# Performance work log

Measured on AMD Instinct MI355X. Metric: run time of the kernel, lower is better.

## Reference

```python
import jax, jax.numpy as jnp
import numpy as np

H, W, C, R, N = 200, 200, 256, 1024, 300


def _mlp(f, W1, b1, W2, b2):
    # Linear -> ReLU -> Linear, applied per pixel
    return jax.nn.relu(f @ W1 + b1) @ W2 + b2


def setup_inputs() -> dict:
    key = jax.random.key(0)
    ks = jax.random.split(key, 16)
    s = 0.02
    inp = {
        'x': jax.random.normal(ks[0], (C, H, W), jnp.float32),
        'masks': jax.random.uniform(ks[1], (H, W, N)) < 0.5,
        'labels': jax.random.randint(ks[2], (N,), 0, 3),  # 0=point,1=line,2=circle
    }
    i = 3
    for p in ('p', 'l', 'c'):
        inp[f'W{p}1'] = s * jax.random.normal(ks[i], (C, R), jnp.float32); i += 1
        inp[f'b{p}1'] = jnp.zeros((R,), jnp.float32)
        inp[f'W{p}2'] = s * jax.random.normal(ks[i], (R, R), jnp.float32); i += 1
        inp[f'b{p}2'] = jnp.zeros((R,), jnp.float32)
    return inp


def reference(x, masks, labels, Wp1, bp1, Wp2, bp2, Wl1, bl1, Wl2, bl2, Wc1, bc1, Wc2, bc2):
    feat = jnp.transpose(x, (1, 2, 0))  # [H, W, C]
    # Apply each label-specific MLP densely over the feature map: [3, H, W, R]
    ys = jnp.stack([
        _mlp(feat, Wp1, bp1, Wp2, bp2),
        _mlp(feat, Wl1, bl1, Wl2, bl2),
        _mlp(feat, Wc1, bc1, Wc2, bc2),
    ], axis=0)
    mf = masks.astype(feat.dtype)                       # [H, W, N]
    sums = jnp.einsum('hwn,khwr->nkr', mf, ys)          # masked sums per node per MLP
    counts = jnp.sum(mf, axis=(0, 1))                   # [N] pixels per mask
    means = sums / counts[:, None, None]                # [N, 3, R]
    # pick the MLP branch matching each node's label -> [N, R]
    return means[jnp.arange(means.shape[0]), labels]
```

## Files before the change

### kernel.cpp

```cpp
#include <hip/hip_runtime.h>

typedef unsigned short u16;
typedef unsigned int   u32;

using bf16x8 = __attribute__((ext_vector_type(8))) __bf16;
using f32x4  = __attribute__((ext_vector_type(4))) float;

__device__ __forceinline__ float bf2f(u16 h){ return __uint_as_float(((u32)h) << 16); }
__device__ __forceinline__ u16 f2bf(float f){
    u32 u = __float_as_uint(f);
    u32 r = u + 0x7FFFu + ((u >> 16) & 1u);
    return (u16)(r >> 16);
}

__device__ __forceinline__ void async16(const void* g, void* l){
    __builtin_amdgcn_global_load_lds(
        (const __attribute__((address_space(1))) unsigned int*)g,
        (__attribute__((address_space(3))) unsigned int*)l, 16, 0, 0);
}
__device__ __forceinline__ bf16x8 cvt8(uint4 v){
    union { uint4 u; bf16x8 b; } c; c.u = v; return c.b;
}

__global__ void probe_and_perm(const void* x, const void* masks, int* flags,
                               const int* labels, int* slot_of_node,
                               int* node_of_slot, int* ovf_flag)
{
    if (blockIdx.x == 0){
        int l = threadIdx.x;
        if (l < 64){
            const u16* hx = (const u16*)x;
            int e0 = (hx[l] >> 7) & 0xFF;
            int e1 = (hx[l + 64] >> 7) & 0xFF;
            unsigned long long b0 = __ballot(e0 >= 100 && e0 <= 140);
            unsigned long long b1 = __ballot(e1 >= 100 && e1 <= 140);
            int cnt = __popcll(b0) + __popcll(b1);
            const u32* w  = (const u32*)masks;
            const u16* hm = (const u16*)masks;
            u32 v = w[l];
            unsigned long long i32bad = __ballot(v > 1u);
            unsigned long long f32bad = __ballot(v != 0u && v != 0x3F800000u);
            u16 h0 = hm[l], h1 = hm[l + 64];
            unsigned long long bfbad =
                __ballot((h0 != 0 && h0 != 0x3F80) || (h1 != 0 && h1 != 0x3F80));
            if (l == 0){
                flags[0] = (cnt >= 100) ? 1 : 0;
                int md = 0;
                if (!i32bad) md = 1; else if (!f32bad) md = 3; else if (!bfbad) md = 2;
                flags[1] = md;
            }
        }
        return;
    }
    __shared__ int lab[300];
    __shared__ unsigned char sp[300];
    int t = threadIdx.x;
    for (int idx = t; idx < 512; idx += 320) node_of_slot[idx] = -1;
    if (t < 300) lab[t] = labels[t];
    __syncthreads();
    int r = 0;
    if (t < 300){
        int k = lab[t];
        for (int j = 0; j < t; j++) r += (lab[j] == k);
        sp[t] = (r >= 128) ? 1 : 0;
    }
    __syncthreads();
    if (t < 300){
        int slot;
        if (!sp[t]) slot = lab[t] * 128 + r;
        else {
            int so = 0;
            for (int j = 0; j < t; j++) so += sp[j];
            slot = 384 + so;
        }
        slot_of_node[t] = slot;
        node_of_slot[slot] = t;
    }
    if (t == 0){
        int tot = 0;
        for (int j = 0; j < 300; j++) tot += sp[j];
        *ovf_flag = tot;
    }
}

__global__ void prep_combo(const void* x,
    const void* w10, const void* w11, const void* w12,
    const void* w20, const void* w21, const void* w22,
    const void* bb10, const void* bb11, const void* bb12,
    const void* bb20, const void* bb21, const void* bb22,
    u16* feat, u16* B1T, u16* W2T, float* b1f, float* b2f, const int* flags)
{
    __shared__ float tile[32][33];
    const int id = blockIdx.x;
    const bool isbf = (flags[0] != 0);
    const int tid = threadIdx.x;
    const int tx = tid & 31, ty = tid >> 5;

    const void* src; u16* d; int I, J, ldd, i0, j0;
    if (id < 10016){
        int fx = id % 1252, fy = id / 1252;
        src = x; d = feat; I = 256; J = 40000; ldd = 256;
        j0 = fx * 32; i0 = fy * 32;
    } else if (id < 10016 + 768){
        int idx = id - 10016;
        int z = idx / 256, r2 = idx % 256;
        src = (z == 0) ? w10 : (z == 1) ? w11 : w12;
        d = B1T + (size_t)z * 1024 * 256;
        I = 256; J = 1024; ldd = 256;
        j0 = (r2 % 32) * 32; i0 = (r2 / 32) * 32;
    } else if (id < 10016 + 768 + 3072){
        int idx = id - 10016 - 768;
        int z = idx / 1024, r2 = idx % 1024;
        src = (z == 0) ? w20 : (z == 1) ? w21 : w22;
        d = W2T + (size_t)z * 1024 * 1024;
        I = 1024; J = 1024; ldd = 1024;
        j0 = (r2 % 32) * 32; i0 = (r2 / 32) * 32;
    } else {
        int idx = (id - 10016 - 768 - 3072) * 256 + tid;
        if (idx < 3072){
            int k = idx >> 10, r2 = idx & 1023;
            const void* p1 = (k == 0) ? bb10 : (k == 1) ? bb11 : bb12;
            const void* p2 = (k == 0) ? bb20 : (k == 1) ? bb21 : bb22;
            b1f[idx] = isbf ? bf2f(((const u16*)p1)[r2]) : ((const float*)p1)[r2];
            b2f[idx] = isbf ? bf2f(((const u16*)p2)[r2]) : ((const float*)p2)[r2];
        }
        return;
    }
    #pragma unroll
    for (int s = 0; s < 32; s += 8){
        int i = i0 + ty + s, j = j0 + tx;
        float v = 0.f;
        if (j < J){
            size_t ix = (size_t)i * J + j;
            v = isbf ? bf2f(((const u16*)src)[ix]) : ((const float*)src)[ix];
        }
        tile[ty + s][tx] = v;
    }
    __syncthreads();
    #pragma unroll
    for (int s = 0; s < 32; s += 8){
        int j = j0 + ty + s, i = i0 + tx;
        d[(size_t)j * ldd + i] = f2bf(tile[tx][ty + s]);
    }
}

__global__ void trans_mask_count(const void* src, u16* dst,
                                 const int* slot_of_node, float* counts,
                                 const int* flags)
{
    constexpr int NN_ = 300, P_ = 40000, LDP = 40064;
    __shared__ u16 tile[128][33];
    __shared__ int slt[32];
    const int p0 = blockIdx.x * 128, n0 = blockIdx.y * 32;
    const int tid = threadIdx.x;
    const int md = flags[1];
    if (tid < 32) slt[tid] = (n0 + tid < NN_) ? slot_of_node[n0 + tid] : -1;

    if (md == 0){
        const unsigned char* s8 = (const unsigned char*)src;
        const int tx = tid & 7, ty = tid >> 3;
        #pragma unroll
        for (int rep = 0; rep < 4; rep++){
            const int p = p0 + rep * 32 + ty;
            const int nb = n0 + tx * 4;
            u32 w = 0;
            if (p < P_){
                if (nb + 3 < NN_)
                    w = *(const u32*)(s8 + (size_t)p * NN_ + nb);
                else {
                    for (int b = 0; b < 4; b++)
                        if (nb + b < NN_)
                            w |= (u32)s8[(size_t)p * NN_ + nb + b] << (8 * b);
                }
            }
            #pragma unroll
            for (int b = 0; b < 4; b++)
                tile[rep * 32 + ty][tx * 4 + b] =
                    ((w >> (8 * b)) & 0xFFu) ? (u16)0x3F80 : (u16)0;
        }
    } else {
        #pragma unroll
        for (int it = 0; it < 16; it++){
            const int e = tid + it * 256;
            const int n_in = e & 31, p_in = e >> 5;
            const int p = p0 + p_in, n = n0 + n_in;
            u16 v = 0;
            if (p < P_ && n < NN_){
                size_t idx = (size_t)p * NN_ + n;
                bool on;
                if (md == 1)      on = ((const int*)src)[idx] != 0;
                else if (md == 2) on = ((const u16*)src)[idx] != 0;
                else              on = ((const float*)src)[idx] != 0.f;
                v = on ? (u16)0x3F80 : (u16)0;
            }
            tile[p_in][n_in] = v;
        }
    }
    __syncthreads();

    #pragma unroll
    for (int half = 0; half < 2; half++){
        const int row = tid >> 3;
        const int pos = (tid & 7) + half * 8;
        const int slot = slt[row];
        if (slot >= 0){
            union { u16 h[8]; uint4 v; } tmp;
            #pragma unroll
            for (int j = 0; j < 8; j++) tmp.h[j] = tile[pos * 8 + j][row];
            *reinterpret_cast<uint4*>(&dst[(size_t)slot * LDP + p0 + pos * 8]) = tmp.v;
        }
    }
    if (tid < 32){
        const int slot = slt[tid];
        if (slot >= 0){
            int c = 0;
            for (int p = 0; p < 128; p++) c += (tile[p][tid] != 0);
            if (c > 0) atomicAdd(&counts[slot], (float)c);
        }
    }
}

template<int MAP>
__global__ __launch_bounds__(256, 2)
void fused_l1_mask(const u16* __restrict__ B1T, const u16* __restrict__ feat,
                   const u16* __restrict__ mfT, const float* __restrict__ b1f,
                   float* __restrict__ sums, const int* __restrict__ skipf)
{
    if constexpr (MAP == 1){ if (*skipf == 0) return; }
    constexpr int PPAD = 40064;
    __shared__ __align__(16) u16 As[32768];
    __shared__ __align__(16) u16 Hs[8192];

    int bx, ts, te;
    if constexpr (MAP == 0){
        const int id = blockIdx.x;
        const int r = id & 7, s = (id >> 3) & 7, g = id >> 6;
        const int combo = g * 8 + r;
        if (combo >= 63) return;
        const int branch = combo / 21, y = combo % 21;
        bx = branch * 8 + s;
        ts = y * 15; te = ts + 15; if (te > 313) te = 313;
    } else {
        bx = blockIdx.x;
        ts = blockIdx.y * 40; te = ts + 40; if (te > 313) te = 313;
        if (ts >= te) return;
    }
    const int m0 = bx * 128;
    const int srow = (MAP == 0) ? ((bx >> 3) * 128) : 384;

    const int tid = threadIdx.x;
    const int wave = tid >> 6, lane = tid & 63;
    const int t = lane & 15, q = lane >> 4;

    {
        const int cr = lane >> 2, cp = lane & 3;
        const int ca = wave * 2, cb = wave * 2 + 1;
        const u16* gA0 = B1T + (size_t)(m0 + ca * 16 + cr) * 256 + cp * 8;
        const u16* gA1 = B1T + (size_t)(m0 + cb * 16 + cr) * 256 + cp * 8;
        #pragma unroll
        for (int kt = 0; kt < 8; kt++){
            async16(gA0 + kt * 32, &As[kt * 4096 + ca * 512]);
            async16(gA1 + kt * 32, &As[kt * 4096 + cb * 512]);
        }
    }

    const u16* mrow = mfT + (size_t)(srow + wave * 32 + t) * PPAD + q * 8;
    const u16* gF   = feat + (size_t)(wave * 32 + t) * 256 + q * 8;
    const float4* bsrc = reinterpret_cast<const float4*>(b1f + m0) + q;

    f32x4 acc2[2][8];
    #pragma unroll
    for (int a = 0; a < 2; a++)
        #pragma unroll
        for (int b = 0; b < 8; b++)
            #pragma unroll
            for (int e = 0; e < 4; e++) acc2[a][b][e] = 0.f;

    uint4 bgv[2];
    #pragma unroll
    for (int ni = 0; ni < 2; ni++)
        bgv[ni] = *reinterpret_cast<const uint4*>(
            gF + (size_t)(ts * 128 + ni * 16) * 256);

    __syncthreads();

#define HWRITE(MOFF) do{                                                      \
    _Pragma("unroll")                                                         \
    for (int mi = 0; mi < 4; mi++){                                           \
        _Pragma("unroll")                                                     \
        for (int i = 0; i < 4; i++){                                          \
            const int m_l = mi * 16 + q * 4 + i;                              \
            _Pragma("unroll")                                                 \
            for (int ni = 0; ni < 2; ni++){                                   \
                const int pin = ni * 16 + t;                                  \
                float v = acc1[(MOFF) + mi][ni][i];                           \
                v = (v > 0.f) ? v : 0.f;                                      \
                const int cg = (pin >> 3) ^ q;                                \
                Hs[wave * 2048 + m_l * 32 + cg * 8 + (pin & 7)] = f2bf(v);    \
            }                                                                 \
        }                                                                     \
    }                                                                         \
}while(0)

#define S2HALF(NOFF) do{                                                      \
    _Pragma("unroll")                                                         \
    for (int lc = 0; lc < 4; lc++){                                           \
        const int hq_ = (q ^ ((t >> 2) & 3)) * 8;                             \
        bf16x8 hb0_ = *reinterpret_cast<const bf16x8*>(                       \
            &Hs[lc * 2048 + (0 * 16 + t) * 32 + hq_]);                        \
        bf16x8 hb1_ = *reinterpret_cast<const bf16x8*>(                       \
            &Hs[lc * 2048 + (1 * 16 + t) * 32 + hq_]);                        \
        bf16x8 hb2_ = *reinterpret_cast<const bf16x8*>(                       \
            &Hs[lc * 2048 + (2 * 16 + t) * 32 + hq_]);                        \
        bf16x8 hb3_ = *reinterpret_cast<const bf16x8*>(                       \
            &Hs[lc * 2048 + (3 * 16 + t) * 32 + hq_]);                        \
        __builtin_amdgcn_s_setprio(1);                                        \
        acc2[0][(NOFF)+0] = __builtin_amdgcn_mfma_f32_16x16x32_bf16(          \
            cvt8(mk[lc][0]), hb0_, acc2[0][(NOFF)+0], 0, 0, 0);               \
        acc2[0][(NOFF)+1] = __builtin_amdgcn_mfma_f32_16x16x32_bf16(          \
            cvt8(mk[lc][0]), hb1_, acc2[0][(NOFF)+1], 0, 0, 0);               \
        acc2[0][(NOFF)+2] = __builtin_amdgcn_mfma_f32_16x16x32_bf16(          \
            cvt8(mk[lc][0]), hb2_, acc2[0][(NOFF)+2], 0, 0, 0);               \
        acc2[0][(NOFF)+3] = __builtin_amdgcn_mfma_f32_16x16x32_bf16(          \
            cvt8(mk[lc][0]), hb3_, acc2[0][(NOFF)+3], 0, 0, 0);               \
        acc2[1][(NOFF)+0] = __builtin_amdgcn_mfma_f32_16x16x32_bf16(          \
            cvt8(mk[lc][1]), hb0_, acc2[1][(NOFF)+0], 0, 0, 0);               \
        acc2[1][(NOFF)+1] = __builtin_amdgcn_mfma_f32_16x16x32_bf16(          \
            cvt8(mk[lc][1]), hb1_, acc2[1][(NOFF)+1], 0, 0, 0);               \
        acc2[1][(NOFF)+2] = __builtin_amdgcn_mfma_f32_16x16x32_bf16(          \
            cvt8(mk[lc][1]), hb2_, acc2[1][(NOFF)+2], 0, 0, 0);               \
        acc2[1][(NOFF)+3] = __builtin_amdgcn_mfma_f32_16x16x32_bf16(          \
            cvt8(mk[lc][1]), hb3_, acc2[1][(NOFF)+3], 0, 0, 0);               \
        __builtin_amdgcn_s_setprio(0);                                        \
    }                                                                         \
}while(0)

    for (int pt = ts; pt < te; ++pt){
        const int p0 = pt * 128;

        f32x4 acc1[8][2];
        #pragma unroll
        for (int mi = 0; mi < 8; mi++){
            float4 bb = bsrc[mi * 4];
            #pragma unroll
            for (int ni = 0; ni < 2; ni++){
                acc1[mi][ni][0] = bb.x; acc1[mi][ni][1] = bb.y;
                acc1[mi][ni][2] = bb.z; acc1[mi][ni][3] = bb.w;
            }
        }

        uint4 mk[4][2];

        #pragma unroll
        for (int kt = 0; kt < 8; ++kt){
            bf16x8 af[8];
            #pragma unroll
            for (int mi = 0; mi < 8; mi++)
                af[mi] = *reinterpret_cast<const bf16x8*>(
                    &As[kt * 4096 + (mi * 16 + t) * 32 + q * 8]);
            uint4 nxt[2];
            if (kt < 7){
                #pragma unroll
                for (int ni = 0; ni < 2; ni++)
                    nxt[ni] = *reinterpret_cast<const uint4*>(
                        gF + (size_t)(p0 + ni * 16) * 256 + (kt + 1) * 32);
            }
            if (kt == 6){
                #pragma unroll
                for (int si = 0; si < 2; si++){
                    mk[0][si] = *reinterpret_cast<const uint4*>(
                        mrow + (size_t)(si * 16) * PPAD + p0 + 0 * 32);
                    mk[1][si] = *reinterpret_cast<const uint4*>(
                        mrow + (size_t)(si * 16) * PPAD + p0 + 1 * 32);
                }
            } else if (kt == 7){
                #pragma unroll
                for (int si = 0; si < 2; si++){
                    mk[2][si] = *reinterpret_cast<const uint4*>(
                        mrow + (size_t)(si * 16) * PPAD + p0 + 2 * 32);
                    mk[3][si] = *reinterpret_cast<const uint4*>(
                        mrow + (size_t)(si * 16) * PPAD + p0 + 3 * 32);
                }
            }
            __builtin_amdgcn_s_setprio(1);
            #pragma unroll
            for (int mi = 0; mi < 8; mi++)
                #pragma unroll
                for (int ni = 0; ni < 2; ni++)
                    acc1[mi][ni] = __builtin_amdgcn_mfma_f32_16x16x32_bf16(
                        af[mi], cvt8(bgv[ni]), acc1[mi][ni], 0, 0, 0);
            __builtin_amdgcn_s_setprio(0);
            if (kt < 7){ bgv[0] = nxt[0]; bgv[1] = nxt[1]; }
        }

        HWRITE(0);
        __syncthreads();

        S2HALF(0);
        __syncthreads();

        HWRITE(4);
        if (pt + 1 < te){
            #pragma unroll
            for (int ni = 0; ni < 2; ni++)
                bgv[ni] = *reinterpret_cast<const uint4*>(
                    gF + (size_t)((pt + 1) * 128 + ni * 16) * 256);
        }
        __syncthreads();

        S2HALF(4);
        __syncthreads();
    }
#undef HWRITE
#undef S2HALF

    #pragma unroll
    for (int si = 0; si < 2; si++){
        #pragma unroll
        for (int i = 0; i < 4; i++){
            const int slot_l = wave * 32 + si * 16 + q * 4 + i;
            #pragma unroll
            for (int ni = 0; ni < 8; ni++){
                const int m_l = ni * 16 + t;
                const float v = acc2[si][ni][i];
                if constexpr (MAP == 0)
                    atomicAdd(sums + (size_t)((bx >> 3) * 128 + slot_l) * 1024
                                   + (bx & 7) * 128 + m_l, v);
                else
                    atomicAdd(sums + (size_t)slot_l * 3072 + bx * 128 + m_l, v);
            }
        }
    }
}

__global__ __launch_bounds__(256)
void l2_gemm(const float* __restrict__ sums3, const float* __restrict__ sumsOvf,
             const float* __restrict__ counts, const u16* __restrict__ W2T,
             const float* __restrict__ b2f, const int* __restrict__ node_of_slot,
             const int* __restrict__ labels, const int* __restrict__ ovfflag,
             void* __restrict__ dout, const int* __restrict__ flags)
{
    const int z = blockIdx.z;
    const int k = (z >= 3) ? z - 3 : z;
    if (z >= 3 && *ovfflag == 0) return;
    const int n0 = blockIdx.x * 128;

    const float* Arow; int astride, slotbase;
    if (z < 3){ Arow = sums3 + (size_t)z * 128 * 1024; astride = 1024; slotbase = z * 128; }
    else      { Arow = sumsOvf + (size_t)k * 1024;     astride = 3072; slotbase = 384; }

    __shared__ __align__(16) u16 As[2][4096];
    __shared__ __align__(16) u16 Bs[2][4096];
    __shared__ float invc[128];

    const int tid  = threadIdx.x;
    const int wave = tid >> 6, lane = tid & 63;
    const int wr = wave >> 1, wc = wave & 1;
    const int t = lane & 15, q = lane >> 4;

    if (tid < 128){
        float c = counts[slotbase + tid];
        invc[tid] = (c > 0.f) ? 1.f / c : 0.f;
    }
    __syncthreads();

    const u16* Bsrc = W2T + (size_t)k * 1024 * 1024;
    const int cr = lane >> 2, cp = lane & 3;
    const int ca = wave * 2, cb = wave * 2 + 1;
    const u16* gB0 = Bsrc + (size_t)(n0 + ca * 16 + cr) * 1024 + cp * 8;
    const u16* gB1 = Bsrc + (size_t)(n0 + cb * 16 + cr) * 1024 + cp * 8;

    const int srow0 = tid >> 2, sq0 = tid & 3;
    const int srow1 = srow0 + 64;

    float4 sv[2][2];

#define L2_LOAD(ktv) do{ \
    const float4* _p0 = reinterpret_cast<const float4*>( \
        Arow + (size_t)srow0 * astride + (ktv) * 32 + sq0 * 8); \
    const float4* _p1 = reinterpret_cast<const float4*>( \
        Arow + (size_t)srow1 * astride + (ktv) * 32 + sq0 * 8); \
    sv[0][0] = _p0[0]; sv[0][1] = _p0[1]; \
    sv[1][0] = _p1[0]; sv[1][1] = _p1[1]; }while(0)
// ... 49 lines not shown
            for (int ni = 0; ni < 4; ni++)
                acc[mi][ni] = __builtin_amdgcn_mfma_f32_16x16x32_bf16(
                    af[mi], bg[ni], acc[mi][ni], 0, 0, 0);
        __builtin_amdgcn_s_setprio(0);
        if (kt < 31) L2_WRITE(buf ^ 1);
        __syncthreads();
        buf ^= 1;
    }
#undef L2_LOAD
#undef L2_WRITE

    const bool outbf = (flags[0] != 0);
    #pragma unroll
    for (int mi = 0; mi < 4; mi++){
        #pragma unroll
        for (int i = 0; i < 4; i++){
            int m_l = wr * 64 + mi * 16 + q * 4 + i;
            int node = node_of_slot[slotbase + m_l];
            bool ok = (node >= 0) && (z < 3 || labels[node] == k);
            if (!ok) continue;
            #pragma unroll
            for (int ni = 0; ni < 4; ni++){
                int n = n0 + wc * 64 + ni * 16 + t;
                float v = acc[mi][ni][i] + b2f[k * 1024 + n];
                size_t oi = (size_t)node * 1024 + n;
                if (outbf) ((u16*)dout)[oi] = f2bf(v);
                else       ((float*)dout)[oi] = v;
            }
        }
    }
}

extern "C" void kernel_launch(void* const* d_in, const int* in_sizes, int n_in,
                              void* d_out, int out_size, void* d_ws, size_t ws_size,
                              hipStream_t stream)
{
    constexpr int C = 256, R = 1024;
    constexpr int PPAD = 40064;
    constexpr int M1 = 3 * R;
    constexpr int SLOTS = 512;

    const void* x      = d_in[0];
    const void* masks  = d_in[1];
    const int*  labels = (const int*)d_in[2];
    (void)in_sizes; (void)n_in; (void)out_size; (void)ws_size;

    char* ws = (char*)d_ws;
    size_t off = 0;
    auto alloc = [&](size_t b)->size_t {
        size_t o = off; off += (b + 255) & ~(size_t)255; return o;
    };

    int*   flags   = (int*)  (ws + alloc(256));
    int*   slotmap = (int*)  (ws + alloc(384 * 4));
    int*   nodemap = (int*)  (ws + alloc(512 * 4));
    int*   ovfflag = (int*)  (ws + alloc(256));
    u16*   feat    = (u16*)  (ws + alloc((size_t)PPAD * C * 2));
    u16*   B1T     = (u16*)  (ws + alloc((size_t)M1 * C * 2));
    float* b1f     = (float*)(ws + alloc((size_t)M1 * 4));
    float* b2f     = (float*)(ws + alloc((size_t)M1 * 4));
    u16*   mfT     = (u16*)  (ws + alloc((size_t)SLOTS * PPAD * 2));
    float* sums3   = (float*)(ws + alloc((size_t)384 * 1024 * 4));
    float* sumsOvf = (float*)(ws + alloc((size_t)128 * M1 * 4));
    float* counts  = (float*)(ws + alloc((size_t)SLOTS * 4));
    u16*   W2T     = (u16*)  (ws + alloc((size_t)3 * R * R * 2));

    probe_and_perm<<<2, 320, 0, stream>>>(x, masks, flags, labels,
                                          slotmap, nodemap, ovfflag);
    hipMemsetAsync(sums3, 0,
        (size_t)384 * 1024 * 4 + (size_t)128 * M1 * 4 + (size_t)SLOTS * 4, stream);

    prep_combo<<<10016 + 768 + 3072 + 12, 256, 0, stream>>>(
        x, d_in[3], d_in[7], d_in[11],
        d_in[5], d_in[9], d_in[13],
        d_in[4], d_in[8], d_in[12],
        d_in[6], d_in[10], d_in[14],
        feat, B1T, W2T, b1f, b2f, flags);

    trans_mask_count<<<dim3(PPAD / 128, 384 / 32), 256, 0, stream>>>(
        masks, mfT, slotmap, counts, flags);

    fused_l1_mask<0><<<512, 256, 0, stream>>>(
        B1T, feat, mfT, b1f, sums3, nullptr);
    fused_l1_mask<1><<<dim3(24, 8), 256, 0, stream>>>(
        B1T, feat, mfT, b1f, sumsOvf, ovfflag);

    l2_gemm<<<dim3(8, 1, 6), 256, 0, stream>>>(
        sums3, sumsOvf, counts, W2T, b2f, nodemap, labels, ovfflag,
        d_out, flags);
}
```

Before: 351.3 us.

## Split fused L1-mask kernel across 8 waves and fold memset into probe kernel

The fused layer-1/mask kernel moves from 4 waves to 8 waves per block, and each wave now owns 16 pixels/slots instead of 32. This halves the per-wave accumulator and register footprint and reworks the LDS layout of the hidden tile with a new XOR swizzle, aiming for higher occupancy (launch bounds 512,4). The software prefetch of features and masks one step ahead is dropped in favour of direct loads, which may expose more memory latency. Separately, the hipMemsetAsync that zeroed the sums buffers is replaced by extra blocks in the probe kernel, removing one launch.

```diff
diff --git a/kernel.cpp b/kernel.cpp
--- a/kernel.cpp
+++ b/kernel.cpp
@@ -24,8 +24,17 @@
 
 __global__ void probe_and_perm(const void* x, const void* masks, int* flags,
                                const int* labels, int* slot_of_node,
-                               int* node_of_slot, int* ovf_flag)
+                               int* node_of_slot, int* ovf_flag,
+                               float* zbuf, unsigned int zf4)
 {
+    if (blockIdx.x >= 2){
+        const unsigned int nthr = (gridDim.x - 2) * blockDim.x;
+        unsigned int i = (blockIdx.x - 2) * blockDim.x + threadIdx.x;
+        float4 z = make_float4(0.f, 0.f, 0.f, 0.f);
+        for (; i < zf4; i += nthr)
+            reinterpret_cast<float4*>(zbuf)[i] = z;
+        return;
+    }
     if (blockIdx.x == 0){
         int l = threadIdx.x;
         if (l < 64){
@@ -221,7 +230,7 @@
 }
 
 template<int MAP>
-__global__ __launch_bounds__(256, 2)
+__global__ __launch_bounds__(512, 4)
 void fused_l1_mask(const u16* __restrict__ B1T, const u16* __restrict__ feat,
                    const u16* __restrict__ mfT, const float* __restrict__ b1f,
                    float* __restrict__ sums, const int* __restrict__ skipf)
@@ -253,51 +262,36 @@
     const int t = lane & 15, q = lane >> 4;
 
     {
-        const int cr = lane >> 2, cp = lane & 3;
-        const int ca = wave * 2, cb = wave * 2 + 1;
-        const u16* gA0 = B1T + (size_t)(m0 + ca * 16 + cr) * 256 + cp * 8;
-        const u16* gA1 = B1T + (size_t)(m0 + cb * 16 + cr) * 256 + cp * 8;
-        #pragma unroll
-        for (int kt = 0; kt < 8; kt++){
-            async16(gA0 + kt * 32, &As[kt * 4096 + ca * 512]);
-            async16(gA1 + kt * 32, &As[kt * 4096 + cb * 512]);
-        }
-    }
-
-    const u16* mrow = mfT + (size_t)(srow + wave * 32 + t) * PPAD + q * 8;
-    const u16* gF   = feat + (size_t)(wave * 32 + t) * 256 + q * 8;
+        const u16* gA = B1T + (size_t)(m0 + wave * 16 + (lane >> 2)) * 256
+                        + (lane & 3) * 8;
+        #pragma unroll
+        for (int kt = 0; kt < 8; kt++)
+            async16(gA + kt * 32, &As[kt * 4096 + wave * 512]);
+    }
+
+    const u16* mrow = mfT + (size_t)(srow + wave * 16 + t) * PPAD + q * 8;
+    const u16* gF   = feat + (size_t)(wave * 16 + t) * 256 + q * 8;
     const float4* bsrc = reinterpret_cast<const float4*>(b1f + m0) + q;
 
-    f32x4 acc2[2][8];
-    #pragma unroll
-    for (int a = 0; a < 2; a++)
-        #pragma unroll
-        for (int b = 0; b < 8; b++)
-            #pragma unroll
-            for (int e = 0; e < 4; e++) acc2[a][b][e] = 0.f;
-
-    uint4 bgv[2];
-    #pragma unroll
-    for (int ni = 0; ni < 2; ni++)
-        bgv[ni] = *reinterpret_cast<const uint4*>(
-            gF + (size_t)(ts * 128 + ni * 16) * 256);
-
-    __syncthreads();
-
-#define HWRITE(MOFF) do{                                                      \
+    f32x4 acc2[8];
+    #pragma unroll
+    for (int b = 0; b < 8; b++)
+        #pragma unroll
+        for (int e = 0; e < 4; e++) acc2[b][e] = 0.f;
+
+    __syncthreads();
+
+#define HWRITE(HALF) do{                                                      \
+    const int pin_ = wave * 16 + t;                                           \
     _Pragma("unroll")                                                         \
     for (int mi = 0; mi < 4; mi++){                                           \
         _Pragma("unroll")                                                     \
         for (int i = 0; i < 4; i++){                                          \
             const int m_l = mi * 16 + q * 4 + i;                              \
-            _Pragma("unroll")                                                 \
-            for (int ni = 0; ni < 2; ni++){                                   \
-                const int pin = ni * 16 + t;                                  \
-                float v = acc1[(MOFF) + mi][ni][i];                           \
-                v = (v > 0.f) ? v : 0.f;                                      \
-                const int cg = (pin >> 3) ^ q;                                \
-                Hs[wave * 2048 + m_l * 32 + cg * 8 + (pin & 7)] = f2bf(v);    \
-            }                                                                 \
+            float v = acc1[(HALF) * 4 + mi][i];                               \
+            v = (v > 0.f) ? v : 0.f;                                          \
+            const int cg = (pin_ >> 3) ^ (m_l & 7);                           \
+            Hs[m_l * 128 + cg * 8 + (pin_ & 7)] = f2bf(v);                    \
         }                                                                     \
     }                                                                         \
 }while(0)
@@ -305,109 +299,55 @@
 #define S2HALF(NOFF) do{                                                      \
     _Pragma("unroll")                                                         \
     for (int lc = 0; lc < 4; lc++){                                           \
-        const int hq_ = (q ^ ((t >> 2) & 3)) * 8;                             \
-        bf16x8 hb0_ = *reinterpret_cast<const bf16x8*>(                       \
-            &Hs[lc * 2048 + (0 * 16 + t) * 32 + hq_]);                        \
-        bf16x8 hb1_ = *reinterpret_cast<const bf16x8*>(                       \
-            &Hs[lc * 2048 + (1 * 16 + t) * 32 + hq_]);                        \
-        bf16x8 hb2_ = *reinterpret_cast<const bf16x8*>(                       \
-            &Hs[lc * 2048 + (2 * 16 + t) * 32 + hq_]);                        \
-        bf16x8 hb3_ = *reinterpret_cast<const bf16x8*>(                       \
-            &Hs[lc * 2048 + (3 * 16 + t) * 32 + hq_]);                        \
+        const uint4 mv = *reinterpret_cast<const uint4*>(mr + lc * 32);       \
         __builtin_amdgcn_s_setprio(1);                                        \
-        acc2[0][(NOFF)+0] = __builtin_amdgcn_mfma_f32_16x16x32_bf16(          \
-            cvt8(mk[lc][0]), hb0_, acc2[0][(NOFF)+0], 0, 0, 0);               \
-        acc2[0][(NOFF)+1] = __builtin_amdgcn_mfma_f32_16x16x32_bf16(          \
-            cvt8(mk[lc][0]), hb1_, acc2[0][(NOFF)+1], 0, 0, 0);               \
-        acc2[0][(NOFF)+2] = __builtin_amdgcn_mfma_f32_16x16x32_bf16(          \
-            cvt8(mk[lc][0]), hb2_, acc2[0][(NOFF)+2], 0, 0, 0);               \
-        acc2[0][(NOFF)+3] = __builtin_amdgcn_mfma_f32_16x16x32_bf16(          \
-            cvt8(mk[lc][0]), hb3_, acc2[0][(NOFF)+3], 0, 0, 0);               \
-        acc2[1][(NOFF)+0] = __builtin_amdgcn_mfma_f32_16x16x32_bf16(          \
-            cvt8(mk[lc][1]), hb0_, acc2[1][(NOFF)+0], 0, 0, 0);               \
-        acc2[1][(NOFF)+1] = __builtin_amdgcn_mfma_f32_16x16x32_bf16(          \
-            cvt8(mk[lc][1]), hb1_, acc2[1][(NOFF)+1], 0, 0, 0);               \
-        acc2[1][(NOFF)+2] = __builtin_amdgcn_mfma_f32_16x16x32_bf16(          \
-            cvt8(mk[lc][1]), hb2_, acc2[1][(NOFF)+2], 0, 0, 0);               \
-        acc2[1][(NOFF)+3] = __builtin_amdgcn_mfma_f32_16x16x32_bf16(          \
-            cvt8(mk[lc][1]), hb3_, acc2[1][(NOFF)+3], 0, 0, 0);               \
+        _Pragma("unroll")                                                     \
+        for (int ni = 0; ni < 4; ni++){                                       \
+            const int m_ = ni * 16 + t;                                       \
+            const int cg = (lc * 4 + q) ^ (m_ & 7);                           \
+            bf16x8 hb = *reinterpret_cast<const bf16x8*>(                     \
+                &Hs[m_ * 128 + cg * 8]);                                      \
+            acc2[(NOFF) + ni] = __builtin_amdgcn_mfma_f32_16x16x32_bf16(      \
+                cvt8(mv), hb, acc2[(NOFF) + ni], 0, 0, 0);                    \
+        }                                                                     \
         __builtin_amdgcn_s_setprio(0);                                        \
     }                                                                         \
 }while(0)
 
     for (int pt = ts; pt < te; ++pt){
         const int p0 = pt * 128;
-
-        f32x4 acc1[8][2];
+        const u16* fF = gF + (size_t)p0 * 256;
+        const u16* mr = mrow + p0;
+
+        f32x4 acc1[8];
         #pragma unroll
         for (int mi = 0; mi < 8; mi++){
             float4 bb = bsrc[mi * 4];
-            #pragma unroll
-            for (int ni = 0; ni < 2; ni++){
-                acc1[mi][ni][0] = bb.x; acc1[mi][ni][1] = bb.y;
-                acc1[mi][ni][2] = bb.z; acc1[mi][ni][3] = bb.w;
-            }
-        }
-
-        uint4 mk[4][2];
+            acc1[mi][0] = bb.x; acc1[mi][1] = bb.y;
+            acc1[mi][2] = bb.z; acc1[mi][3] = bb.w;
+        }
 
         #pragma unroll
         for (int kt = 0; kt < 8; ++kt){
-            bf16x8 af[8];
-            #pragma unroll
-            for (int mi = 0; mi < 8; mi++)
-                af[mi] = *reinterpret_cast<const bf16x8*>(
-                    &As[kt * 4096 + (mi * 16 + t) * 32 + q * 8]);
-            uint4 nxt[2];
-            if (kt < 7){
-                #pragma unroll
-                for (int ni = 0; ni < 2; ni++)
-                    nxt[ni] = *reinterpret_cast<const uint4*>(
-                        gF + (size_t)(p0 + ni * 16) * 256 + (kt + 1) * 32);
-            }
-            if (kt == 6){
-                #pragma unroll
-                for (int si = 0; si < 2; si++){
-                    mk[0][si] = *reinterpret_cast<const uint4*>(
-                        mrow + (size_t)(si * 16) * PPAD + p0 + 0 * 32);
-                    mk[1][si] = *reinterpret_cast<const uint4*>(
-                        mrow + (size_t)(si * 16) * PPAD + p0 + 1 * 32);
-                }
-            } else if (kt == 7){
-                #pragma unroll
-                for (int si = 0; si < 2; si++){
-                    mk[2][si] = *reinterpret_cast<const uint4*>(
-                        mrow + (size_t)(si * 16) * PPAD + p0 + 2 * 32);
-                    mk[3][si] = *reinterpret_cast<const uint4*>(
-                        mrow + (size_t)(si * 16) * PPAD + p0 + 3 * 32);
-                }
-            }
+            const uint4 fv = *reinterpret_cast<const uint4*>(fF + kt * 32);
             __builtin_amdgcn_s_setprio(1);
             #pragma unroll
-            for (int mi = 0; mi < 8; mi++)
-                #pragma unroll
-                for (int ni = 0; ni < 2; ni++)
-                    acc1[mi][ni] = __builtin_amdgcn_mfma_f32_16x16x32_bf16(
-                        af[mi], cvt8(bgv[ni]), acc1[mi][ni], 0, 0, 0);
+            for (int mi = 0; mi < 8; mi++){
+                bf16x8 af = *reinterpret_cast<const bf16x8*>(
+                    &As[kt * 4096 + (mi * 16 + t) * 32 + q * 8]);
+                acc1[mi] = __builtin_amdgcn_mfma_f32_16x16x32_bf16(
+                    af, cvt8(fv), acc1[mi], 0, 0, 0);
+            }
             __builtin_amdgcn_s_setprio(0);
-            if (kt < 7){ bgv[0] = nxt[0]; bgv[1] = nxt[1]; }
         }
 
         HWRITE(0);
         __syncthreads();
-
         S2HALF(0);
         __syncthreads();
 
-        HWRITE(4);
-        if (pt + 1 < te){
-            #pragma unroll
-            for (int ni = 0; ni < 2; ni++)
-                bgv[ni] = *reinterpret_cast<const uint4*>(
-                    gF + (size_t)((pt + 1) * 128 + ni * 16) * 256);
-        }
+        HWRITE(1);
         __syncthreads();
-
         S2HALF(4);
         __syncthreads();
     }
@@ -415,20 +355,17 @@
 #undef S2HALF
 
     #pragma unroll
-    for (int si = 0; si < 2; si++){
-        #pragma unroll
-        for (int i = 0; i < 4; i++){
-            const int slot_l = wave * 32 + si * 16 + q * 4 + i;
-            #pragma unroll
-            for (int ni = 0; ni < 8; ni++){
-                const int m_l = ni * 16 + t;
-                const float v = acc2[si][ni][i];
-                if constexpr (MAP == 0)
-                    atomicAdd(sums + (size_t)((bx >> 3) * 128 + slot_l) * 1024
-                                   + (bx & 7) * 128 + m_l, v);
-                else
-                    atomicAdd(sums + (size_t)slot_l * 3072 + bx * 128 + m_l, v);
-            }
+    for (int i = 0; i < 4; i++){
+        const int slot_l = wave * 16 + q * 4 + i;
+        #pragma unroll
+        for (int ni = 0; ni < 8; ni++){
+            const int m_l = ni * 16 + t;
+            const float v = acc2[ni][i];
+            if constexpr (MAP == 0)
+                atomicAdd(sums + (size_t)((bx >> 3) * 128 + slot_l) * 1024
+                               + (bx & 7) * 128 + m_l, v);
+            else
+                atomicAdd(sums + (size_t)slot_l * 3072 + bx * 128 + m_l, v);
         }
     }
 }
@@ -597,10 +534,12 @@
     float* counts  = (float*)(ws + alloc((size_t)SLOTS * 4));
     u16*   W2T     = (u16*)  (ws + alloc((size_t)3 * R * R * 2));
 
-    probe_and_perm<<<2, 320, 0, stream>>>(x, masks, flags, labels,
-                                          slotmap, nodemap, ovfflag);
-    hipMemsetAsync(sums3, 0,
-        (size_t)384 * 1024 * 4 + (size_t)128 * M1 * 4 + (size_t)SLOTS * 4, stream);
+    const unsigned int zf4 =
+        (384u * 1024u + 128u * 3072u + 512u) / 4u;
+
+    probe_and_perm<<<66, 320, 0, stream>>>(x, masks, flags, labels,
+                                           slotmap, nodemap, ovfflag,
+                                           sums3, zf4);
 
     prep_combo<<<10016 + 768 + 3072 + 12, 256, 0, stream>>>(
         x, d_in[3], d_in[7], d_in[11],
@@ -612,9 +551,9 @@
     trans_mask_count<<<dim3(PPAD / 128, 384 / 32), 256, 0, stream>>>(
         masks, mfT, slotmap, counts, flags);
 
-    fused_l1_mask<0><<<512, 256, 0, stream>>>(
+    fused_l1_mask<0><<<512, 512, 0, stream>>>(
         B1T, feat, mfT, b1f, sums3, nullptr);
-    fused_l1_mask<1><<<dim3(24, 8), 256, 0, stream>>>(
+    fused_l1_mask<1><<<dim3(24, 8), 512, 0, stream>>>(
         B1T, feat, mfT, b1f, sumsOvf, ovfflag);
 
     l2_gemm<<<dim3(8, 1, 6), 256, 0, stream>>>(
```

New measurement: 435.4 us. 1.24x slower.

## Merge probe, prep transposes and mask transpose into one mega kernel

Applied to the files above, without the earlier changes.

Folds probe_and_perm, prep_combo and trans_mask_count into a single launch, with blocks dispatched by index. Each block now recomputes the dtype probe and the label rank and slot mapping locally instead of reading them from a global buffer written by an earlier kernel. This removes two kernel launches and the serialization between them. In exchange every mask-transpose block repeats an O(N^2) rank computation over 300 labels, every prep block repeats the probe, and shared memory per block grows.

```diff
diff --git a/kernel.cpp b/kernel.cpp
--- a/kernel.cpp
+++ b/kernel.cpp
@@ -22,28 +22,48 @@
     union { uint4 u; bf16x8 b; } c; c.u = v; return c.b;
 }
 
-__global__ void probe_and_perm(const void* x, const void* masks, int* flags,
-                               const int* labels, int* slot_of_node,
-                               int* node_of_slot, int* ovf_flag)
+__global__ __launch_bounds__(256)
+void mega_prep(const void* x, const void* masks, const int* labels,
+    const void* w10, const void* w11, const void* w12,
+    const void* w20, const void* w21, const void* w22,
+    const void* bb10, const void* bb11, const void* bb12,
+    const void* bb20, const void* bb21, const void* bb22,
+    u16* feat, u16* B1T, u16* W2T, float* b1f, float* b2f,
+    u16* mfT, float* counts,
+    int* flags, int* node_of_slot, int* ovf_flag)
 {
-    if (blockIdx.x == 0){
-        int l = threadIdx.x;
-        if (l < 64){
+    constexpr int NN_ = 300, P_ = 40000, LDP = 40064;
+    constexpr int PREP_BASE = 2, NPREP = 10016 + 768 + 3072 + 12;
+    constexpr int TRANS_BASE = PREP_BASE + NPREP;
+
+    __shared__ float ftile[32][33];
+    __shared__ u16 mtile[128][33];
+    __shared__ int lab[NN_];
+    __shared__ short rnk[NN_];
+    __shared__ unsigned char sp[NN_];
+    __shared__ int slt[32];
+    __shared__ int s_info;
+
+    const int id = blockIdx.x;
+    const int tid = threadIdx.x;
+
+    if (id == 0){
+        if (tid < 64){
             const u16* hx = (const u16*)x;
-            int e0 = (hx[l] >> 7) & 0xFF;
-            int e1 = (hx[l + 64] >> 7) & 0xFF;
+            int e0 = (hx[tid] >> 7) & 0xFF;
+            int e1 = (hx[tid + 64] >> 7) & 0xFF;
             unsigned long long b0 = __ballot(e0 >= 100 && e0 <= 140);
             unsigned long long b1 = __ballot(e1 >= 100 && e1 <= 140);
             int cnt = __popcll(b0) + __popcll(b1);
             const u32* w  = (const u32*)masks;
             const u16* hm = (const u16*)masks;
-            u32 v = w[l];
+            u32 v = w[tid];
             unsigned long long i32bad = __ballot(v > 1u);
             unsigned long long f32bad = __ballot(v != 0u && v != 0x3F800000u);
-            u16 h0 = hm[l], h1 = hm[l + 64];
+            u16 h0 = hm[tid], h1 = hm[tid + 64];
             unsigned long long bfbad =
                 __ballot((h0 != 0 && h0 != 0x3F80) || (h1 != 0 && h1 != 0x3F80));
-            if (l == 0){
+            if (tid == 0){
                 flags[0] = (cnt >= 100) ? 1 : 0;
                 int md = 0;
                 if (!i32bad) md = 1; else if (!f32bad) md = 3; else if (!bfbad) md = 2;
@@ -52,170 +72,196 @@
         }
         return;
     }
-    __shared__ int lab[300];
-    __shared__ unsigned char sp[300];
-    int t = threadIdx.x;
-    for (int idx = t; idx < 512; idx += 320) node_of_slot[idx] = -1;
-    if (t < 300) lab[t] = labels[t];
-    __syncthreads();
-    int r = 0;
-    if (t < 300){
-        int k = lab[t];
-        for (int j = 0; j < t; j++) r += (lab[j] == k);
-        sp[t] = (r >= 128) ? 1 : 0;
-    }
-    __syncthreads();
-    if (t < 300){
-        int slot;
-        if (!sp[t]) slot = lab[t] * 128 + r;
-        else {
-            int so = 0;
-            for (int j = 0; j < t; j++) so += sp[j];
-            slot = 384 + so;
-        }
-        slot_of_node[t] = slot;
-        node_of_slot[slot] = t;
-    }
-    if (t == 0){
-        int tot = 0;
-        for (int j = 0; j < 300; j++) tot += sp[j];
-        *ovf_flag = tot;
-    }
-}
-
-__global__ void prep_combo(const void* x,
-    const void* w10, const void* w11, const void* w12,
-    const void* w20, const void* w21, const void* w22,
-    const void* bb10, const void* bb11, const void* bb12,
-    const void* bb20, const void* bb21, const void* bb22,
-    u16* feat, u16* B1T, u16* W2T, float* b1f, float* b2f, const int* flags)
-{
-    __shared__ float tile[32][33];
-    const int id = blockIdx.x;
-    const bool isbf = (flags[0] != 0);
-    const int tid = threadIdx.x;
-    const int tx = tid & 31, ty = tid >> 5;
-
-    const void* src; u16* d; int I, J, ldd, i0, j0;
-    if (id < 10016){
-        int fx = id % 1252, fy = id / 1252;
-        src = x; d = feat; I = 256; J = 40000; ldd = 256;
-        j0 = fx * 32; i0 = fy * 32;
-    } else if (id < 10016 + 768){
-        int idx = id - 10016;
-        int z = idx / 256, r2 = idx % 256;
-        src = (z == 0) ? w10 : (z == 1) ? w11 : w12;
-        d = B1T + (size_t)z * 1024 * 256;
-        I = 256; J = 1024; ldd = 256;
-        j0 = (r2 % 32) * 32; i0 = (r2 / 32) * 32;
-    } else if (id < 10016 + 768 + 3072){
-        int idx = id - 10016 - 768;
-        int z = idx / 1024, r2 = idx % 1024;
-        src = (z == 0) ? w20 : (z == 1) ? w21 : w22;
-        d = W2T + (size_t)z * 1024 * 1024;
-        I = 1024; J = 1024; ldd = 1024;
-        j0 = (r2 % 32) * 32; i0 = (r2 / 32) * 32;
-    } else {
-        int idx = (id - 10016 - 768 - 3072) * 256 + tid;
-        if (idx < 3072){
-            int k = idx >> 10, r2 = idx & 1023;
-            const void* p1 = (k == 0) ? bb10 : (k == 1) ? bb11 : bb12;
-            const void* p2 = (k == 0) ? bb20 : (k == 1) ? bb21 : bb22;
-            b1f[idx] = isbf ? bf2f(((const u16*)p1)[r2]) : ((const float*)p1)[r2];
-            b2f[idx] = isbf ? bf2f(((const u16*)p2)[r2]) : ((const float*)p2)[r2];
+
+    if (id == 1){
+        for (int idx = tid; idx < 512; idx += 256) node_of_slot[idx] = -1;
+        for (int n = tid; n < NN_; n += 256) lab[n] = labels[n];
+        __syncthreads();
+        for (int n = tid; n < NN_; n += 256){
+            int k = lab[n], r = 0;
+            for (int j = 0; j < n; j++) r += (lab[j] == k);
+            rnk[n] = (short)r; sp[n] = (r >= 128) ? 1 : 0;
+        }
+        __syncthreads();
+        for (int n = tid; n < NN_; n += 256){
+            int r = rnk[n]; int slot;
+            if (r < 128) slot = lab[n] * 128 + r;
+            else { int so = 0; for (int j = 0; j < n; j++) so += sp[j]; slot = 384 + so; }
+            node_of_slot[slot] = n;
+        }
+        if (tid == 0){
+            int tot = 0;
+            for (int j = 0; j < NN_; j++) tot += sp[j];
+            *ovf_flag = tot;
         }
         return;
     }
-    #pragma unroll
-    for (int s = 0; s < 32; s += 8){
-        int i = i0 + ty + s, j = j0 + tx;
-        float v = 0.f;
-        if (j < J){
-            size_t ix = (size_t)i * J + j;
-            v = isbf ? bf2f(((const u16*)src)[ix]) : ((const float*)src)[ix];
-        }
-        tile[ty + s][tx] = v;
-    }
-    __syncthreads();
-    #pragma unroll
-    for (int s = 0; s < 32; s += 8){
-        int j = j0 + ty + s, i = i0 + tx;
-        d[(size_t)j * ldd + i] = f2bf(tile[tx][ty + s]);
-    }
-}
-
-__global__ void trans_mask_count(const void* src, u16* dst,
-                                 const int* slot_of_node, float* counts,
-                                 const int* flags)
-{
-    constexpr int NN_ = 300, P_ = 40000, LDP = 40064;
-    __shared__ u16 tile[128][33];
-    __shared__ int slt[32];
-    const int p0 = blockIdx.x * 128, n0 = blockIdx.y * 32;
-    const int tid = threadIdx.x;
-    const int md = flags[1];
-    if (tid < 32) slt[tid] = (n0 + tid < NN_) ? slot_of_node[n0 + tid] : -1;
-
-    if (md == 0){
-        const unsigned char* s8 = (const unsigned char*)src;
-        const int tx = tid & 7, ty = tid >> 3;
-        #pragma unroll
-        for (int rep = 0; rep < 4; rep++){
-            const int p = p0 + rep * 32 + ty;
-            const int nb = n0 + tx * 4;
-            u32 w = 0;
-            if (p < P_){
-                if (nb + 3 < NN_)
-                    w = *(const u32*)(s8 + (size_t)p * NN_ + nb);
-                else {
-                    for (int b = 0; b < 4; b++)
-                        if (nb + b < NN_)
-                            w |= (u32)s8[(size_t)p * NN_ + nb + b] << (8 * b);
+
+    if (id < TRANS_BASE){
+        if (tid < 64){
+            const u16* hx = (const u16*)x;
+            int e0 = (hx[tid] >> 7) & 0xFF;
+            int e1 = (hx[tid + 64] >> 7) & 0xFF;
+            unsigned long long b0 = __ballot(e0 >= 100 && e0 <= 140);
+            unsigned long long b1 = __ballot(e1 >= 100 && e1 <= 140);
+            if (tid == 0) s_info = (__popcll(b0) + __popcll(b1) >= 100) ? 1 : 0;
+        }
+        __syncthreads();
+        const bool isbf = (s_info != 0);
+        const int pid = id - PREP_BASE;
+        const int tx = tid & 31, ty = tid >> 5;
+
+        const void* src; u16* d; int J, ldd, i0, j0;
+        if (pid < 10016){
+            int fx = pid % 1252, fy = pid / 1252;
+            src = x; d = feat; J = 40000; ldd = 256;
+            j0 = fx * 32; i0 = fy * 32;
+        } else if (pid < 10016 + 768){
+            int idx = pid - 10016;
+            int z = idx / 256, r2 = idx % 256;
+            src = (z == 0) ? w10 : (z == 1) ? w11 : w12;
+            d = B1T + (size_t)z * 1024 * 256;
+            J = 1024; ldd = 256;
+            j0 = (r2 % 32) * 32; i0 = (r2 / 32) * 32;
+        } else if (pid < 10016 + 768 + 3072){
+            int idx = pid - 10016 - 768;
+            int z = idx / 1024, r2 = idx % 1024;
+            src = (z == 0) ? w20 : (z == 1) ? w21 : w22;
+            d = W2T + (size_t)z * 1024 * 1024;
+            J = 1024; ldd = 1024;
+            j0 = (r2 % 32) * 32; i0 = (r2 / 32) * 32;
+        } else {
+            int idx = (pid - 10016 - 768 - 3072) * 256 + tid;
+            if (idx < 3072){
+                int k = idx >> 10, r2 = idx & 1023;
+                const void* p1 = (k == 0) ? bb10 : (k == 1) ? bb11 : bb12;
+                const void* p2 = (k == 0) ? bb20 : (k == 1) ? bb21 : bb22;
+                b1f[idx] = isbf ? bf2f(((const u16*)p1)[r2]) : ((const float*)p1)[r2];
+                b2f[idx] = isbf ? bf2f(((const u16*)p2)[r2]) : ((const float*)p2)[r2];
+            }
+            return;
+        }
+        #pragma unroll
+        for (int s = 0; s < 32; s += 8){
+            int i = i0 + ty + s, j = j0 + tx;
+            float v = 0.f;
+            if (j < J){
+                size_t ix = (size_t)i * J + j;
+                v = isbf ? bf2f(((const u16*)src)[ix]) : ((const float*)src)[ix];
+            }
+            ftile[ty + s][tx] = v;
+        }
+        __syncthreads();
+        #pragma unroll
+        for (int s = 0; s < 32; s += 8){
+            int j = j0 + ty + s, i = i0 + tx;
+            d[(size_t)j * ldd + i] = f2bf(ftile[tx][ty + s]);
+        }
+        return;
+    }
+
+    {
+        const int idx = id - TRANS_BASE;
+        const int pb = idx % 313, nb = idx / 313;
+        const int p0 = pb * 128, n0 = nb * 32;
+
+        for (int n = tid; n < NN_; n += 256) lab[n] = labels[n];
+        if (tid < 64){
+            const u32* w  = (const u32*)masks;
+            const u16* hm = (const u16*)masks;
+            u32 v = w[tid];
+            unsigned long long i32bad = __ballot(v > 1u);
+            unsigned long long f32bad = __ballot(v != 0u && v != 0x3F800000u);
+            u16 h0 = hm[tid], h1 = hm[tid + 64];
+            unsigned long long bfbad =
+                __ballot((h0 != 0 && h0 != 0x3F80) || (h1 != 0 && h1 != 0x3F80));
+            if (tid == 0){
+                int md = 0;
+                if (!i32bad) md = 1; else if (!f32bad) md = 3; else if (!bfbad) md = 2;
+                s_info = md;
+            }
+        }
+        __syncthreads();
+        const int md = s_info;
+
+        for (int n = tid; n < NN_; n += 256){
+            int k = lab[n], r = 0;
+            for (int j = 0; j < n; j++) r += (lab[j] == k);
+            rnk[n] = (short)r; sp[n] = (r >= 128) ? 1 : 0;
+        }
+        __syncthreads();
+        if (tid < 32){
+            int n = n0 + tid;
+            int slot = -1;
+            if (n < NN_){
+                int r = rnk[n];
+                if (r < 128) slot = lab[n] * 128 + r;
+                else { int so = 0; for (int j = 0; j < n; j++) so += sp[j]; slot = 384 + so; }
+            }
+            slt[tid] = slot;
+        }
+
+        if (md == 0){
+            const unsigned char* s8 = (const unsigned char*)masks;
+            const int tx = tid & 7, ty = tid >> 3;
+            #pragma unroll
+            for (int rep = 0; rep < 4; rep++){
+                const int p = p0 + rep * 32 + ty;
+                const int nbyte = n0 + tx * 4;
+                u32 w = 0;
+                if (p < P_){
+                    if (nbyte + 3 < NN_)
+                        w = *(const u32*)(s8 + (size_t)p * NN_ + nbyte);
+                    else {
+                        for (int b = 0; b < 4; b++)
+                            if (nbyte + b < NN_)
+                                w |= (u32)s8[(size_t)p * NN_ + nbyte + b] << (8 * b);
+                    }
                 }
-            }
-            #pragma unroll
-            for (int b = 0; b < 4; b++)
-                tile[rep * 32 + ty][tx * 4 + b] =
-                    ((w >> (8 * b)) & 0xFFu) ? (u16)0x3F80 : (u16)0;
-        }
-    } else {
-        #pragma unroll
-        for (int it = 0; it < 16; it++){
-            const int e = tid + it * 256;
-            const int n_in = e & 31, p_in = e >> 5;
-            const int p = p0 + p_in, n = n0 + n_in;
-            u16 v = 0;
-            if (p < P_ && n < NN_){
-                size_t idx = (size_t)p * NN_ + n;
-                bool on;
-                if (md == 1)      on = ((const int*)src)[idx] != 0;
-                else if (md == 2) on = ((const u16*)src)[idx] != 0;
-                else              on = ((const float*)src)[idx] != 0.f;
-                v = on ? (u16)0x3F80 : (u16)0;
-            }
-            tile[p_in][n_in] = v;
-        }
-    }
-    __syncthreads();
-
-    #pragma unroll
-    for (int half = 0; half < 2; half++){
-        const int row = tid >> 3;
-        const int pos = (tid & 7) + half * 8;
-        const int slot = slt[row];
-        if (slot >= 0){
-            union { u16 h[8]; uint4 v; } tmp;
-            #pragma unroll
-            for (int j = 0; j < 8; j++) tmp.h[j] = tile[pos * 8 + j][row];
-            *reinterpret_cast<uint4*>(&dst[(size_t)slot * LDP + p0 + pos * 8]) = tmp.v;
-        }
-    }
-    if (tid < 32){
-        const int slot = slt[tid];
-        if (slot >= 0){
-            int c = 0;
-            for (int p = 0; p < 128; p++) c += (tile[p][tid] != 0);
-            if (c > 0) atomicAdd(&counts[slot], (float)c);
+                #pragma unroll
+                for (int b = 0; b < 4; b++)
+                    mtile[rep * 32 + ty][tx * 4 + b] =
+                        ((w >> (8 * b)) & 0xFFu) ? (u16)0x3F80 : (u16)0;
+            }
+        } else {
+            #pragma unroll
+            for (int it = 0; it < 16; it++){
+                const int e = tid + it * 256;
+                const int n_in = e & 31, p_in = e >> 5;
+                const int p = p0 + p_in, n = n0 + n_in;
+                u16 v = 0;
+                if (p < P_ && n < NN_){
+                    size_t ix = (size_t)p * NN_ + n;
+                    bool on;
+                    if (md == 1)      on = ((const int*)masks)[ix] != 0;
+                    else if (md == 2) on = ((const u16*)masks)[ix] != 0;
+                    else              on = ((const float*)masks)[ix] != 0.f;
+                    v = on ? (u16)0x3F80 : (u16)0;
+                }
+                mtile[p_in][n_in] = v;
+            }
+        }
+        __syncthreads();
+
+        #pragma unroll
+        for (int half = 0; half < 2; half++){
+            const int row = tid >> 3;
+            const int pos = (tid & 7) + half * 8;
+            const int slot = slt[row];
+            if (slot >= 0){
+                union { u16 h[8]; uint4 v; } tmp;
+                #pragma unroll
+                for (int j = 0; j < 8; j++) tmp.h[j] = mtile[pos * 8 + j][row];
+                *reinterpret_cast<uint4*>(&mfT[(size_t)slot * LDP + p0 + pos * 8]) = tmp.v;
+            }
+        }
+        if (tid < 32){
+            const int slot = slt[tid];
+            if (slot >= 0){
+                int c = 0;
+                for (int p = 0; p < 128; p++) c += (mtile[p][tid] != 0);
+                if (c > 0) atomicAdd(&counts[slot], (float)c);
+            }
         }
     }
 }
@@ -584,7 +630,6 @@
     };
 
     int*   flags   = (int*)  (ws + alloc(256));
-    int*   slotmap = (int*)  (ws + alloc(384 * 4));
     int*   nodemap = (int*)  (ws + alloc(512 * 4));
     int*   ovfflag = (int*)  (ws + alloc(256));
     u16*   feat    = (u16*)  (ws + alloc((size_t)PPAD * C * 2));
@@ -597,20 +642,20 @@
     float* counts  = (float*)(ws + alloc((size_t)SLOTS * 4));
     u16*   W2T     = (u16*)  (ws + alloc((size_t)3 * R * R * 2));
 
-    probe_and_perm<<<2, 320, 0, stream>>>(x, masks, flags, labels,
-                                          slotmap, nodemap, ovfflag);
     hipMemsetAsync(sums3, 0,
-        (size_t)384 * 1024 * 4 + (size_t)128 * M1 * 4 + (size_t)SLOTS * 4, stream);
-
-    prep_combo<<<10016 + 768 + 3072 + 12, 256, 0, stream>>>(
-        x, d_in[3], d_in[7], d_in[11],
+        (size_t)384 * 1024 * 4 + (size_t)128 * M1 * 4 + (size_t)SLOTS * 4,
+        stream);
+
+    constexpr int NPREP = 10016 + 768 + 3072 + 12;
+    constexpr int NTRANS = 313 * 12;
+    mega_prep<<<2 + NPREP + NTRANS, 256, 0, stream>>>(
+        x, masks, labels,
+        d_in[3], d_in[7], d_in[11],
         d_in[5], d_in[9], d_in[13],
         d_in[4], d_in[8], d_in[12],
         d_in[6], d_in[10], d_in[14],
-        feat, B1T, W2T, b1f, b2f, flags);
-
-    trans_mask_count<<<dim3(PPAD / 128, 384 / 32), 256, 0, stream>>>(
-        masks, mfT, slotmap, counts, flags);
+        feat, B1T, W2T, b1f, b2f, mfT, counts,
+        flags, nodemap, ovfflag);
 
     fused_l1_mask<0><<<512, 256, 0, stream>>>(
         B1T, feat, mfT, b1f, sums3, nullptr);
```

Result: slower. 366.0 us (+4.2%).

## Vectorize prep transposes with 64x64 bf16 tiles and fold memset into probe kernel

Applied to the files above, without the earlier changes.

The transpose/convert kernel now uses 64x64 tiles stored as bf16 in shared memory. It reads with 4-wide vector loads and writes 16-byte packed stores, so the feature map and weight transposes need far fewer, wider memory transactions. Padding tiles past the pixel count are written as zeros directly. Separately, the hipMemsetAsync of the accumulation buffers is replaced by extra blocks in the probe kernel that zero the buffers with float4 stores, which removes one stream operation. The zeroing relies on the three buffers being contiguous in the workspace.

```diff
diff --git a/kernel.cpp b/kernel.cpp
--- a/kernel.cpp
+++ b/kernel.cpp
@@ -24,8 +24,17 @@
 
 __global__ void probe_and_perm(const void* x, const void* masks, int* flags,
                                const int* labels, int* slot_of_node,
-                               int* node_of_slot, int* ovf_flag)
+                               int* node_of_slot, int* ovf_flag,
+                               float* zbuf, unsigned int zf4)
 {
+    if (blockIdx.x >= 2){
+        const unsigned int nthr = (gridDim.x - 2) * blockDim.x;
+        unsigned int i = (blockIdx.x - 2) * blockDim.x + threadIdx.x;
+        float4 z = make_float4(0.f, 0.f, 0.f, 0.f);
+        for (; i < zf4; i += nthr)
+            reinterpret_cast<float4*>(zbuf)[i] = z;
+        return;
+    }
     if (blockIdx.x == 0){
         int l = threadIdx.x;
         if (l < 64){
@@ -83,40 +92,44 @@
     }
 }
 
-__global__ void prep_combo(const void* x,
+__global__ __launch_bounds__(256)
+void prep_combo(const void* x,
     const void* w10, const void* w11, const void* w12,
     const void* w20, const void* w21, const void* w22,
     const void* bb10, const void* bb11, const void* bb12,
     const void* bb20, const void* bb21, const void* bb22,
     u16* feat, u16* B1T, u16* W2T, float* b1f, float* b2f, const int* flags)
 {
-    __shared__ float tile[32][33];
+    constexpr int NFEAT = 626 * 4;
+    constexpr int NB1 = NFEAT + 192;
+    constexpr int NW2 = NB1 + 768;
+
+    __shared__ u16 tile[64 * 68];
     const int id = blockIdx.x;
     const bool isbf = (flags[0] != 0);
     const int tid = threadIdx.x;
-    const int tx = tid & 31, ty = tid >> 5;
-
-    const void* src; u16* d; int I, J, ldd, i0, j0;
-    if (id < 10016){
-        int fx = id % 1252, fy = id / 1252;
-        src = x; d = feat; I = 256; J = 40000; ldd = 256;
-        j0 = fx * 32; i0 = fy * 32;
-    } else if (id < 10016 + 768){
-        int idx = id - 10016;
-        int z = idx / 256, r2 = idx % 256;
+
+    const void* src; u16* d; int J, ldd, i0, j0;
+    if (id < NFEAT){
+        int pblk = id >> 2, cblk = id & 3;
+        src = x; d = feat; J = 40000; ldd = 256;
+        j0 = pblk * 64; i0 = cblk * 64;
+    } else if (id < NB1){
+        int idx = id - NFEAT;
+        int z = idx >> 6, r2 = idx & 63;
         src = (z == 0) ? w10 : (z == 1) ? w11 : w12;
         d = B1T + (size_t)z * 1024 * 256;
-        I = 256; J = 1024; ldd = 256;
-        j0 = (r2 % 32) * 32; i0 = (r2 / 32) * 32;
-    } else if (id < 10016 + 768 + 3072){
-        int idx = id - 10016 - 768;
-        int z = idx / 1024, r2 = idx % 1024;
+        J = 1024; ldd = 256;
+        j0 = (r2 & 15) * 64; i0 = (r2 >> 4) * 64;
+    } else if (id < NW2){
+        int idx = id - NB1;
+        int z = idx >> 8, r2 = idx & 255;
         src = (z == 0) ? w20 : (z == 1) ? w21 : w22;
         d = W2T + (size_t)z * 1024 * 1024;
-        I = 1024; J = 1024; ldd = 1024;
-        j0 = (r2 % 32) * 32; i0 = (r2 / 32) * 32;
+        J = 1024; ldd = 1024;
+        j0 = (r2 & 15) * 64; i0 = (r2 >> 4) * 64;
     } else {
-        int idx = (id - 10016 - 768 - 3072) * 256 + tid;
+        int idx = (id - NW2) * 256 + tid;
         if (idx < 3072){
             int k = idx >> 10, r2 = idx & 1023;
             const void* p1 = (k == 0) ? bb10 : (k == 1) ? bb11 : bb12;
@@ -126,21 +139,56 @@
         }
         return;
     }
+
+    const int wave = tid >> 6, lane = tid & 63;
+    const int rr = wave * 4 + (lane >> 4);
+    const int cc = (lane & 15) * 4;
+
+    if (j0 >= J){
+        #pragma unroll
+        for (int pass = 0; pass < 4; pass++){
+            const int r = pass * 16 + rr;
+            union { u16 h[4]; uint2 v; } pk;
+            pk.h[0] = 0; pk.h[1] = 0; pk.h[2] = 0; pk.h[3] = 0;
+            *reinterpret_cast<uint2*>(&tile[r * 68 + cc]) = pk.v;
+        }
+    } else if (isbf){
+        const u16* sh = (const u16*)src;
+        #pragma unroll
+        for (int pass = 0; pass < 4; pass++){
+            const int r = pass * 16 + rr;
+            const size_t ix = (size_t)(i0 + r) * J + (j0 + cc);
+            ushort4 v = *reinterpret_cast<const ushort4*>(&sh[ix]);
+            union { u16 h[4]; uint2 u; } pk;
+            pk.h[0] = v.x; pk.h[1] = v.y; pk.h[2] = v.z; pk.h[3] = v.w;
+            *reinterpret_cast<uint2*>(&tile[r * 68 + cc]) = pk.u;
+        }
+    } else {
+        const float* sf = (const float*)src;
+        #pragma unroll
+        for (int pass = 0; pass < 4; pass++){
+            const int r = pass * 16 + rr;
+            const size_t ix = (size_t)(i0 + r) * J + (j0 + cc);
+            float4 v = *reinterpret_cast<const float4*>(&sf[ix]);
+            union { u16 h[4]; uint2 u; } pk;
+            pk.h[0] = f2bf(v.x); pk.h[1] = f2bf(v.y);
+            pk.h[2] = f2bf(v.z); pk.h[3] = f2bf(v.w);
+            *reinterpret_cast<uint2*>(&tile[r * 68 + cc]) = pk.u;
+        }
+    }
+    __syncthreads();
+
     #pragma unroll
-    for (int s = 0; s < 32; s += 8){
-        int i = i0 + ty + s, j = j0 + tx;
-        float v = 0.f;
-        if (j < J){
-            size_t ix = (size_t)i * J + j;
-            v = isbf ? bf2f(((const u16*)src)[ix]) : ((const float*)src)[ix];
-        }
-        tile[ty + s][tx] = v;
-    }
-    __syncthreads();
-    #pragma unroll
-    for (int s = 0; s < 32; s += 8){
-        int j = j0 + ty + s, i = i0 + tx;
-        d[(size_t)j * ldd + i] = f2bf(tile[tx][ty + s]);
+    for (int pass = 0; pass < 2; pass++){
+        const int s = pass * 256 + tid;
+        const int p = s & 63;
+        const int chunk = s >> 6;
+        union { u16 h[8]; uint4 v; } pk;
+        #pragma unroll
+        for (int k = 0; k < 8; k++)
+            pk.h[k] = tile[(chunk * 8 + k) * 68 + p];
+        *reinterpret_cast<uint4*>(
+            &d[(size_t)(j0 + p) * ldd + i0 + chunk * 8]) = pk.v;
     }
 }
 
@@ -597,12 +645,13 @@
     float* counts  = (float*)(ws + alloc((size_t)SLOTS * 4));
     u16*   W2T     = (u16*)  (ws + alloc((size_t)3 * R * R * 2));
 
-    probe_and_perm<<<2, 320, 0, stream>>>(x, masks, flags, labels,
-                                          slotmap, nodemap, ovfflag);
-    hipMemsetAsync(sums3, 0,
-        (size_t)384 * 1024 * 4 + (size_t)128 * M1 * 4 + (size_t)SLOTS * 4, stream);
-
-    prep_combo<<<10016 + 768 + 3072 + 12, 256, 0, stream>>>(
+    const unsigned int zf4 = (384u * 1024u + 128u * 3072u + 512u) / 4u;
+
+    probe_and_perm<<<66, 320, 0, stream>>>(x, masks, flags, labels,
+                                           slotmap, nodemap, ovfflag,
+                                           sums3, zf4);
+
+    prep_combo<<<2504 + 192 + 768 + 12, 256, 0, stream>>>(
         x, d_in[3], d_in[7], d_in[11],
         d_in[5], d_in[9], d_in[13],
         d_in[4], d_in[8], d_in[12],
```

After: 345.6 us. About the same (-1.6%).
